# Performance work log

Measured on AMD Instinct MI355X. Metric: run time of the kernel, lower is better.

## Reference

```python
import jax, jax.numpy as jnp
import numpy as np

B, D, H = 16384, 1024, 4096


def setup_inputs() -> dict:
    key = jax.random.key(0)
    kx, kp, k1, k2 = jax.random.split(key, 4)
    X = jax.random.normal(kx, (B, D), dtype=jnp.float32)
    prot_col_idx = 3
    # protected column must be binary {0,1} so the remap produces no NaNs
    prot = jax.random.randint(kp, (B,), 0, 2).astype(jnp.float32)
    X = X.at[:, prot_col_idx].set(prot)
    W1 = jax.random.normal(k1, (D, H), dtype=jnp.float32) * (1.0 / np.sqrt(D))
    b1 = jnp.zeros((H,), dtype=jnp.float32)
    W2 = jax.random.normal(k2, (H, D), dtype=jnp.float32) * (1.0 / np.sqrt(H))
    b2 = jnp.zeros((D,), dtype=jnp.float32)
    return {"X": X, "W1": W1, "b1": b1, "W2": W2, "b2": b2,
            "prot_col_idx": prot_col_idx}


def reference(X, W1, b1, W2, b2, prot_col_idx):
    def explainer(x):
        h = jnp.tanh(x @ W1 + b1)          # [B, H]
        return h @ W2 + b2                  # [B, D]

    # vectorized remap of the protected column: 0 -> 1, 1 -> 0, else NaN
    col = X[:, prot_col_idx]
    flipped = jnp.where(col == 0, jnp.float32(1.0),
                        jnp.where(col == 1, jnp.float32(0.0), jnp.float32(jnp.nan)))
    X_copy = X.at[:, prot_col_idx].set(flipped.astype(X.dtype))

    shaps = explainer(X)
    shaps_counter = explainer(X_copy)
    mean_euclid_dist = jnp.mean(jnp.abs(shaps - shaps_counter), axis=0)  # [D]
    return mean_euclid_dist.sum()
```

## Files before the change

### kernel.cpp

```cpp
#include <hip/hip_runtime.h>
#include <stdint.h>

#define B_N 16384
#define D_N 1024
#define H_N 4096

typedef int i32x4 __attribute__((ext_vector_type(4)));
typedef int i32x8 __attribute__((ext_vector_type(8)));
typedef float f32x4 __attribute__((ext_vector_type(4)));

__device__ __forceinline__ void gload16(const void* g, void* l) {
  __builtin_amdgcn_global_load_lds((const __attribute__((address_space(1))) void*)g,
                                   (__attribute__((address_space(3))) void*)l,
                                   16, 0, 0);
}

__device__ __forceinline__ unsigned char f2fp8(float v) {
  return (unsigned char)(__builtin_amdgcn_cvt_pk_fp8_f32(v, v, 0, false) & 0xFF);
}

__device__ __forceinline__ void transpose_tile(
    const float* __restrict__ in, unsigned char* __restrict__ out,
    int R, int C, float scale, float* __restrict__ w3, int pci,
    int i0, int j0, int tx, int ty) {
  __shared__ float tile[32][33];
#pragma unroll
  for (int r = 0; r < 32; r += 8) {
    int i = i0 + ty + r;
    int j = j0 + tx;
    float v = in[(size_t)i * C + j];
    tile[ty + r][tx] = v;
    if (w3 != nullptr && i == pci) w3[j] = v;
  }
  __syncthreads();
#pragma unroll
  for (int r = 0; r < 32; r += 8) {
    int jo = j0 + ty + r;
    int io = i0 + tx;
    out[(size_t)jo * R + io] = f2fp8(tile[tx][ty + r] * scale);
  }
}

__global__ __launch_bounds__(256) void prep_kernel(
    const float4* __restrict__ X4, int* __restrict__ Xb,
    float* __restrict__ s,
    const float* __restrict__ W1, unsigned char* __restrict__ W1T, float* __restrict__ w3,
    const float* __restrict__ W2, unsigned char* __restrict__ W2T,
    const int* __restrict__ pci_p) {
  int b = blockIdx.x;
  int tid = threadIdx.x;
  int pci = *pci_p;
  if (b < 16384) {
    int i = b * 256 + tid;
    float4 v = X4[i];
    int p = __builtin_amdgcn_cvt_pk_fp8_f32(v.x, v.y, 0, false);
    p = __builtin_amdgcn_cvt_pk_fp8_f32(v.z, v.w, p, true);
    Xb[i] = p;
    int colg = i & (D_N / 4 - 1);
    if (colg == (pci >> 2)) {
      int row = i >> 8;
      float c;
      switch (pci & 3) {
        case 0:  c = v.x; break;
        case 1:  c = v.y; break;
        case 2:  c = v.z; break;
        default: c = v.w; break;
      }
      s[row] = 1.0f - 2.0f * c;
    }
  } else if (b < 20480) {
    int id = b - 16384;
    transpose_tile(W1, W1T, D_N, H_N, 16.0f, w3, pci,
                   (id >> 7) * 32, (id & 127) * 32, tid & 31, tid >> 5);
  } else {
    int id = b - 20480;
    transpose_tile(W2, W2T, H_N, D_N, 64.0f, nullptr, -1,
                   (id >> 5) * 32, (id & 31) * 32, tid & 31, tid >> 5);
  }
}

template <int KTOT>
__device__ __forceinline__ void mx_mainloop(
    const unsigned char* __restrict__ A, const unsigned char* __restrict__ B,
    int m0, int n0, int sa, int sb,
    unsigned char* As, unsigned char* Bs, f32x4 (&acc)[4][4]) {
  const int tid = threadIdx.x;
  const int lane = tid & 63;
  const int wave = tid >> 6;
  const int wm = (wave >> 1) * 64;
  const int wn = (wave & 1) * 64;
  const int lm = lane & 15;
  const int quad = lane >> 4;

  const int srow = tid >> 3;
  const int clog = (tid & 7) ^ (srow & 7);
  const unsigned char* Ag = A + (size_t)(m0 + srow) * KTOT + clog * 16;
  const unsigned char* Bg = B + (size_t)(n0 + srow) * KTOT + clog * 16;
  unsigned char* As_l = As + tid * 16;
  unsigned char* Bs_l = Bs + tid * 16;

  for (int k0 = 0; k0 < KTOT; k0 += 128) {
#pragma unroll
    for (int it = 0; it < 4; it++) {
      gload16(Ag + k0 + (size_t)(32 * it) * KTOT, As_l + it * 4096);
      gload16(Bg + k0 + (size_t)(32 * it) * KTOT, Bs_l + it * 4096);
    }
    __syncthreads();
    i32x8 a[4], b[4];
#pragma unroll
    for (int i = 0; i < 4; i++) {
      int r = wm + i * 16 + lm;
      int e = r & 7;
      i32x4 lo = *(const i32x4*)&As[r * 128 + ((2 * quad) ^ e) * 16];
      i32x4 hi = *(const i32x4*)&As[r * 128 + ((2 * quad + 1) ^ e) * 16];
      a[i][0] = lo[0]; a[i][1] = lo[1]; a[i][2] = lo[2]; a[i][3] = lo[3];
      a[i][4] = hi[0]; a[i][5] = hi[1]; a[i][6] = hi[2]; a[i][7] = hi[3];
    }
#pragma unroll
    for (int j = 0; j < 4; j++) {
      int r = wn + j * 16 + lm;
      int e = r & 7;
      i32x4 lo = *(const i32x4*)&Bs[r * 128 + ((2 * quad) ^ e) * 16];
      i32x4 hi = *(const i32x4*)&Bs[r * 128 + ((2 * quad + 1) ^ e) * 16];
      b[j][0] = lo[0]; b[j][1] = lo[1]; b[j][2] = lo[2]; b[j][3] = lo[3];
      b[j][4] = hi[0]; b[j][5] = hi[1]; b[j][6] = hi[2]; b[j][7] = hi[3];
    }
#pragma unroll
    for (int i = 0; i < 4; i++)
#pragma unroll
      for (int j = 0; j < 4; j++)
        acc[i][j] = __builtin_amdgcn_mfma_scale_f32_16x16x128_f8f6f4(
            a[i], b[j], acc[i][j], 0, 0, 0, sa, 0, sb);
    __syncthreads();
  }
}

__global__ __launch_bounds__(256) void gemm1_dh(
    const unsigned char* __restrict__ Xb,
    const unsigned char* __restrict__ W1T,
    const float* __restrict__ b1,
    const float* __restrict__ w3,
    const float* __restrict__ s,
    unsigned char* __restrict__ Dh) {
  __shared__ alignas(16) unsigned char As[128 * 128];
  __shared__ alignas(16) unsigned char Bs[128 * 128];
  {
  }
  int l = blockIdx.y * gridDim.x + blockIdx.x;
  int x = l & 7;
  int k = l >> 3;
  int ni = k & 7;
  int m  = (k >> 3) & 15;
  int nc = k >> 7;
  const int m0 = (x * 16 + m) * 128;
  const int n0 = (nc * 8 + ni) * 128;

  f32x4 acc[4][4] = {};
  mx_mainloop<D_N>(Xb, W1T, m0, n0, 127, 123, As, Bs, acc);

  const int tid = threadIdx.x;
  const int lane = tid & 63;
  const int wave = tid >> 6;
  const int wm = (wave >> 1) * 64;
  const int wn = (wave & 1) * 64;
  const int lm = lane & 15;
  const int quad = lane >> 4;

  float ewp[4], ewm[4], nump[4], numm[4], b1v[4];
  int ghv[4];
#pragma unroll
  for (int j = 0; j < 4; j++) {
    int gh = n0 + wn + j * 16 + lm;
    float w = w3[gh];
    float ep = __expf(2.0f * w);
    float em = __expf(-2.0f * w);
    ewp[j] = ep; ewm[j] = em;
    nump[j] = 128.0f * (1.0f - ep);
    numm[j] = 128.0f * (1.0f - em);
    b1v[j] = b1[gh];
    ghv[j] = gh;
  }
#pragma unroll
  for (int i = 0; i < 4; i++) {
#pragma unroll
    for (int r = 0; r < 4; r++) {
      int gb = m0 + wm + i * 16 + quad * 4 + r;
      bool sp = s[gb] > 0.0f;
      size_t rowbase = (size_t)gb * H_N;
      float o[4];
#pragma unroll
      for (int j = 0; j < 4; j++) {
        float ews = sp ? ewp[j] : ewm[j];
        float num = sp ? nump[j] : numm[j];
        float z = fminf(acc[i][j][r] + b1v[j], 12.0f);
        float E = __expf(2.0f * z);
        float den = (E * ews + 1.0f) * (E + 1.0f);
        o[j] = (E * num) * __builtin_amdgcn_rcpf(den);
      }
      int p01 = __builtin_amdgcn_cvt_pk_fp8_f32(o[0], o[1], 0, false);
      int p23 = __builtin_amdgcn_cvt_pk_fp8_f32(o[2], o[3], 0, false);
      Dh[rowbase + ghv[0]] = (unsigned char)(p01 & 0xFF);
      Dh[rowbase + ghv[1]] = (unsigned char)((p01 >> 8) & 0xFF);
      Dh[rowbase + ghv[2]] = (unsigned char)(p23 & 0xFF);
      Dh[rowbase + ghv[3]] = (unsigned char)((p23 >> 8) & 0xFF);
    }
  }
}

__global__ __launch_bounds__(256) void gemm2_abs(
    const unsigned char* __restrict__ Dh,
    const unsigned char* __restrict__ W2T,
    float* __restrict__ out) {
  __shared__ alignas(16) unsigned char As[128 * 128];
  __shared__ alignas(16) unsigned char Bs[128 * 128];
  __shared__ float wsum[4];
  int l = blockIdx.y * gridDim.x + blockIdx.x;
  int x = l & 7;
  int k = l >> 3;
  int ni = k & 7;
  int m  = k >> 3;
  const int m0 = (x * 16 + m) * 128;
  const int n0 = ni * 128;

  f32x4 acc[4][4] = {};
  mx_mainloop<H_N>(Dh, W2T, m0, n0, 121, 121, As, Bs, acc);

  const int tid = threadIdx.x;
  const int lane = tid & 63;
  const int wave = tid >> 6;

  float t = 0.0f;
#pragma unroll
  for (int i = 0; i < 4; i++)
#pragma unroll
    for (int j = 0; j < 4; j++)
#pragma unroll
      for (int r = 0; r < 4; r++)
        t += fabsf(acc[i][j][r]);

#pragma unroll
  for (int off2 = 32; off2 > 0; off2 >>= 1)
    t += __shfl_down(t, off2, 64);
  if (lane == 0) wsum[wave] = t;
  __syncthreads();
  if (tid == 0)
    atomicAdd(out, (wsum[0] + wsum[1] + wsum[2] + wsum[3]) * (1.0f / (float)B_N));
}

extern "C" void kernel_launch(void* const* d_in, const int* in_sizes, int n_in,
                              void* d_out, int out_size, void* d_ws, size_t ws_size,
                              hipStream_t stream) {
  const float* X  = (const float*)d_in[0];
  const float* W1 = (const float*)d_in[1];
  const float* b1 = (const float*)d_in[2];
  const float* W2 = (const float*)d_in[3];
  const int* pci  = (const int*)d_in[5];

  char* ws = (char*)d_ws;
  size_t off = 0;
  unsigned char* Xb  = (unsigned char*)(ws + off); off += (size_t)B_N * D_N;
  unsigned char* W1T = (unsigned char*)(ws + off); off += (size_t)H_N * D_N;
  unsigned char* W2T = (unsigned char*)(ws + off); off += (size_t)D_N * H_N;
  float* w3  = (float*)(ws + off); off += (size_t)H_N * 4;
  float* s   = (float*)(ws + off); off += (size_t)B_N * 4;
  unsigned char* Dh  = (unsigned char*)(ws + off); off += (size_t)B_N * H_N;
  if (ws_size < off) return;

  hipMemsetAsync(d_out, 0, sizeof(float), stream);
  prep_kernel<<<24576, 256, 0, stream>>>((const float4*)X, (int*)Xb, s,
                                         W1, W1T, w3, W2, W2T, pci);
  gemm1_dh<<<dim3(32, 128), 256, 0, stream>>>(Xb, W1T, b1, w3, s, Dh);
  gemm2_abs<<<dim3(8, 128), 256, 0, stream>>>(Dh, W2T, (float*)d_out);
}
```

Baseline: 310.7 us.

## Permute hidden dimension so GEMM1 epilogue writes packed 4-byte fp8 words

Rows of W2T are transposed into a permuted hidden-index order matching the lane layout of the GEMM1 accumulators. Each lane can then pack its four fp8 outputs into one 32-bit store, replacing four scattered byte stores to the large intermediate. Because W2T uses the same permutation, the contraction stays consistent. The change also splits the prep kernel into separate X-pack and transpose kernels, folds the output zeroing into the pack kernel in place of a memset, and remaps GEMM2 block order for better locality.

```diff
diff --git a/kernel.cpp b/kernel.cpp
--- a/kernel.cpp
+++ b/kernel.cpp
@@ -19,46 +19,25 @@
   return (unsigned char)(__builtin_amdgcn_cvt_pk_fp8_f32(v, v, 0, false) & 0xFF);
 }
 
-__device__ __forceinline__ void transpose_tile(
-    const float* __restrict__ in, unsigned char* __restrict__ out,
-    int R, int C, float scale, float* __restrict__ w3, int pci,
-    int i0, int j0, int tx, int ty) {
-  __shared__ float tile[32][33];
-#pragma unroll
-  for (int r = 0; r < 32; r += 8) {
-    int i = i0 + ty + r;
-    int j = j0 + tx;
-    float v = in[(size_t)i * C + j];
-    tile[ty + r][tx] = v;
-    if (w3 != nullptr && i == pci) w3[j] = v;
-  }
-  __syncthreads();
-#pragma unroll
-  for (int r = 0; r < 32; r += 8) {
-    int jo = j0 + ty + r;
-    int io = i0 + tx;
-    out[(size_t)jo * R + io] = f2fp8(tile[tx][ty + r] * scale);
-  }
-}
-
-__global__ __launch_bounds__(256) void prep_kernel(
+__device__ __forceinline__ int perm_h(int h) {
+  return (h & ~63) | ((h & 15) << 2) | ((h >> 4) & 3);
+}
+
+__global__ __launch_bounds__(256) void pack_x_kernel(
     const float4* __restrict__ X4, int* __restrict__ Xb,
-    float* __restrict__ s,
-    const float* __restrict__ W1, unsigned char* __restrict__ W1T, float* __restrict__ w3,
-    const float* __restrict__ W2, unsigned char* __restrict__ W2T,
-    const int* __restrict__ pci_p) {
-  int b = blockIdx.x;
-  int tid = threadIdx.x;
+    float* __restrict__ s, const int* __restrict__ pci_p,
+    float* __restrict__ out0) {
+  int i = (blockIdx.x * 256 + threadIdx.x) * 2;
+  if (blockIdx.x == 0 && threadIdx.x == 0) out0[0] = 0.0f;
   int pci = *pci_p;
-  if (b < 16384) {
-    int i = b * 256 + tid;
-    float4 v = X4[i];
+#pragma unroll
+  for (int u = 0; u < 2; u++) {
+    float4 v = X4[i + u];
     int p = __builtin_amdgcn_cvt_pk_fp8_f32(v.x, v.y, 0, false);
     p = __builtin_amdgcn_cvt_pk_fp8_f32(v.z, v.w, p, true);
-    Xb[i] = p;
-    int colg = i & (D_N / 4 - 1);
-    if (colg == (pci >> 2)) {
-      int row = i >> 8;
+    Xb[i + u] = p;
+    if (((i + u) & (D_N / 4 - 1)) == (pci >> 2)) {
+      int row = (i + u) >> 8;
       float c;
       switch (pci & 3) {
         case 0:  c = v.x; break;
@@ -68,14 +47,46 @@
       }
       s[row] = 1.0f - 2.0f * c;
     }
-  } else if (b < 20480) {
-    int id = b - 16384;
+  }
+}
+
+__device__ __forceinline__ void transpose_tile(
+    const float* __restrict__ in, unsigned char* __restrict__ out,
+    int R, int C, float scale, float* __restrict__ w3, int pci,
+    int i0, int j0, int tx, int ty, bool permute) {
+  __shared__ float tile[32][33];
+#pragma unroll
+  for (int r = 0; r < 32; r += 8) {
+    int i = i0 + ty + r;
+    int j = j0 + tx;
+    float v = in[(size_t)i * C + j];
+    tile[ty + r][tx] = v;
+    if (w3 != nullptr && i == pci) w3[j] = v;
+  }
+  __syncthreads();
+#pragma unroll
+  for (int r = 0; r < 32; r += 8) {
+    int jo = j0 + ty + r;
+    int io = i0 + tx;
+    int ioo = permute ? perm_h(io) : io;
+    out[(size_t)jo * R + ioo] = f2fp8(tile[tx][ty + r] * scale);
+  }
+}
+
+__global__ __launch_bounds__(256) void transpose_kernel(
+    const float* __restrict__ W1, unsigned char* __restrict__ W1T, float* __restrict__ w3,
+    const float* __restrict__ W2, unsigned char* __restrict__ W2T,
+    const int* __restrict__ pci_p) {
+  int b = blockIdx.x;
+  int tid = threadIdx.x;
+  int pci = *pci_p;
+  if (b < 4096) {
     transpose_tile(W1, W1T, D_N, H_N, 16.0f, w3, pci,
-                   (id >> 7) * 32, (id & 127) * 32, tid & 31, tid >> 5);
+                   (b >> 7) * 32, (b & 127) * 32, tid & 31, tid >> 5, false);
   } else {
-    int id = b - 20480;
+    int id = b - 4096;
     transpose_tile(W2, W2T, H_N, D_N, 64.0f, nullptr, -1,
-                   (id >> 5) * 32, (id & 31) * 32, tid & 31, tid >> 5);
+                   (id >> 5) * 32, (id & 31) * 32, tid & 31, tid >> 5, true);
   }
 }
 
@@ -113,8 +124,7 @@
       int e = r & 7;
       i32x4 lo = *(const i32x4*)&As[r * 128 + ((2 * quad) ^ e) * 16];
       i32x4 hi = *(const i32x4*)&As[r * 128 + ((2 * quad + 1) ^ e) * 16];
-      a[i][0] = lo[0]; a[i][1] = lo[1]; a[i][2] = lo[2]; a[i][3] = lo[3];
-      a[i][4] = hi[0]; a[i][5] = hi[1]; a[i][6] = hi[2]; a[i][7] = hi[3];
+      a[i] = __builtin_shufflevector(lo, hi, 0, 1, 2, 3, 4, 5, 6, 7);
     }
 #pragma unroll
     for (int j = 0; j < 4; j++) {
@@ -122,8 +132,7 @@
       int e = r & 7;
       i32x4 lo = *(const i32x4*)&Bs[r * 128 + ((2 * quad) ^ e) * 16];
       i32x4 hi = *(const i32x4*)&Bs[r * 128 + ((2 * quad + 1) ^ e) * 16];
-      b[j][0] = lo[0]; b[j][1] = lo[1]; b[j][2] = lo[2]; b[j][3] = lo[3];
-      b[j][4] = hi[0]; b[j][5] = hi[1]; b[j][6] = hi[2]; b[j][7] = hi[3];
+      b[j] = __builtin_shufflevector(lo, hi, 0, 1, 2, 3, 4, 5, 6, 7);
     }
 #pragma unroll
     for (int i = 0; i < 4; i++)
@@ -141,11 +150,9 @@
     const float* __restrict__ b1,
     const float* __restrict__ w3,
     const float* __restrict__ s,
-    unsigned char* __restrict__ Dh) {
+    unsigned int* __restrict__ Dh4) {
   __shared__ alignas(16) unsigned char As[128 * 128];
   __shared__ alignas(16) unsigned char Bs[128 * 128];
-  {
-  }
   int l = blockIdx.y * gridDim.x + blockIdx.x;
   int x = l & 7;
   int k = l >> 3;
@@ -167,7 +174,6 @@
   const int quad = lane >> 4;
 
   float ewp[4], ewm[4], nump[4], numm[4], b1v[4];
-  int ghv[4];
 #pragma unroll
   for (int j = 0; j < 4; j++) {
     int gh = n0 + wn + j * 16 + lm;
@@ -178,15 +184,14 @@
     nump[j] = 128.0f * (1.0f - ep);
     numm[j] = 128.0f * (1.0f - em);
     b1v[j] = b1[gh];
-    ghv[j] = gh;
-  }
+  }
+  const size_t coloff = (size_t)((n0 + wn) >> 2) + lm;
 #pragma unroll
   for (int i = 0; i < 4; i++) {
 #pragma unroll
     for (int r = 0; r < 4; r++) {
       int gb = m0 + wm + i * 16 + quad * 4 + r;
       bool sp = s[gb] > 0.0f;
-      size_t rowbase = (size_t)gb * H_N;
       float o[4];
 #pragma unroll
       for (int j = 0; j < 4; j++) {
@@ -197,12 +202,9 @@
         float den = (E * ews + 1.0f) * (E + 1.0f);
         o[j] = (E * num) * __builtin_amdgcn_rcpf(den);
       }
-      int p01 = __builtin_amdgcn_cvt_pk_fp8_f32(o[0], o[1], 0, false);
-      int p23 = __builtin_amdgcn_cvt_pk_fp8_f32(o[2], o[3], 0, false);
-      Dh[rowbase + ghv[0]] = (unsigned char)(p01 & 0xFF);
-      Dh[rowbase + ghv[1]] = (unsigned char)((p01 >> 8) & 0xFF);
-      Dh[rowbase + ghv[2]] = (unsigned char)(p23 & 0xFF);
-      Dh[rowbase + ghv[3]] = (unsigned char)((p23 >> 8) & 0xFF);
+      int p = __builtin_amdgcn_cvt_pk_fp8_f32(o[0], o[1], 0, false);
+      p = __builtin_amdgcn_cvt_pk_fp8_f32(o[2], o[3], p, true);
+      Dh4[(size_t)gb * (H_N / 4) + coloff] = (unsigned int)p;
     }
   }
 }
@@ -217,10 +219,12 @@
   int l = blockIdx.y * gridDim.x + blockIdx.x;
   int x = l & 7;
   int k = l >> 3;
-  int ni = k & 7;
-  int m  = k >> 3;
+  int c = k >> 6;
+  int idx = k & 63;
+  int m  = idx >> 2;
+  int nj = idx & 3;
   const int m0 = (x * 16 + m) * 128;
-  const int n0 = ni * 128;
+  const int n0 = (c * 4 + nj) * 128;
 
   f32x4 acc[4][4] = {};
   mx_mainloop<H_N>(Dh, W2T, m0, n0, 121, 121, As, Bs, acc);
@@ -266,9 +270,10 @@
   unsigned char* Dh  = (unsigned char*)(ws + off); off += (size_t)B_N * H_N;
   if (ws_size < off) return;
 
-  hipMemsetAsync(d_out, 0, sizeof(float), stream);
-  prep_kernel<<<24576, 256, 0, stream>>>((const float4*)X, (int*)Xb, s,
-                                         W1, W1T, w3, W2, W2T, pci);
-  gemm1_dh<<<dim3(32, 128), 256, 0, stream>>>(Xb, W1T, b1, w3, s, Dh);
+  pack_x_kernel<<<8192, 256, 0, stream>>>((const float4*)X, (int*)Xb, s, pci,
+                                          (float*)d_out);
+  transpose_kernel<<<8192, 256, 0, stream>>>(W1, W1T, w3, W2, W2T, pci);
+  gemm1_dh<<<dim3(32, 128), 256, 0, stream>>>(Xb, W1T, b1, w3, s,
+                                              (unsigned int*)Dh);
   gemm2_abs<<<dim3(8, 128), 256, 0, stream>>>(Dh, W2T, (float*)d_out);
 }
```

Measured after the change: 309.0 us. No clear change (-0.6%).
